# Kernel tuning notes

Measured on AMD Instinct MI355X. Metric: run time of the kernel, lower is better.

The kernel has to match this reference:

```python
import jax, jax.numpy as jnp
import numpy as np

N = 100_000            # nodes (residues) across batch
E = 1_200_000          # directed edges before duplication
G = 400                # graphs in batch
RBF_SIZE = 16
MIN_D, MAX_D = 0.0, 20.0
RAW_EDGE = 2           # enc_in_edges - rbf_size
RAW_NODE = 51          # enc_in_nodes - residue_emb_size
EMB = 32
NODE_OUT = 2           # features.Output.Node.LENGTH
GLOB_OUT = 1           # features.Output.Global.LENGTH
# (in_e, in_n, out_e, out_n) per message-passing layer (layers=3 schedule)
LAYER_DIMS = [(8, 16, 16, 32), (16, 32, 32, 64), (32, 64, 64, 128)]


def setup_inputs() -> dict:
    key = jax.random.key(0)
    ks = iter(jax.random.split(key, 64))
    def nrm(shape, s=0.1):
        return jax.random.normal(next(ks), shape, jnp.float32) * s
    inp = dict(
        node_raw=nrm((N, RAW_NODE), 1.0),
        edge_raw=nrm((E, RAW_EDGE), 1.0),
        distances=jax.random.uniform(next(ks), (E,), jnp.float32, 0.0, MAX_D),
        residues=jax.random.randint(next(ks), (N,), 0, 22, jnp.int32),
        senders=jax.random.randint(next(ks), (E,), 0, N, jnp.int32),
        receivers=jax.random.randint(next(ks), (E,), 0, N, jnp.int32),
        node_graph_idx=jnp.sort(jax.random.randint(next(ks), (N,), 0, G, jnp.int32)),
        emb=nrm((22, EMB), 1.0),
        enc_We1=nrm((18, 4)), enc_be1=jnp.zeros((4,), jnp.float32),
        enc_We2=nrm((4, 8)), enc_be2=jnp.zeros((8,), jnp.float32),
        enc_Wn1=nrm((83, 8)), enc_bn1=jnp.zeros((8,), jnp.float32),
        enc_Wn2=nrm((8, 16)), enc_bn2=jnp.zeros((16,), jnp.float32),
        ro_Wg=nrm((128, GLOB_OUT)), ro_bg=jnp.zeros((GLOB_OUT,), jnp.float32),
        ro_Wn=nrm((128, NODE_OUT)), ro_bn=jnp.zeros((NODE_OUT,), jnp.float32),
    )
    for i, (ie, inn, oe, on) in enumerate(LAYER_DIMS):
        inp[f'l{i}_We'] = nrm((ie, oe))
        inp[f'l{i}_Ws'] = nrm((inn, oe))
        inp[f'l{i}_be'] = jnp.zeros((oe,), jnp.float32)
        inp[f'l{i}_Wn'] = nrm((inn, on))
        inp[f'l{i}_Wi'] = nrm((oe, on))
        inp[f'l{i}_bn'] = jnp.zeros((on,), jnp.float32)
    return inp


def _seg_mean(x, idx, num):
    s = jax.ops.segment_sum(x, idx, num_segments=num)
    c = jax.ops.segment_sum(jnp.ones((x.shape[0],), x.dtype), idx, num_segments=num)
    return s / jnp.maximum(c, 1.0)[:, None]


def _forward(node_raw, edge_raw, distances, residues, senders, receivers, node_graph_idx,
             emb, enc_We1, enc_be1, enc_We2, enc_be2, enc_Wn1, enc_bn1, enc_Wn2, enc_bn2,
             ro_Wg, ro_bg, ro_Wn, ro_bn, layer_params):
    relu = jax.nn.relu
    # --- preprocessing ---
    centers = jnp.linspace(MIN_D, MAX_D, RBF_SIZE)
    rbf = jnp.exp(-(distances[:, None] - centers[None, :]) ** 2)      # [E, 16]
    ef = jnp.concatenate([rbf, edge_raw], axis=1)                      # [E, 18]
    nf = jnp.concatenate([emb[residues], node_raw], axis=1)            # [N, 83]
    # duplicate (symmetrize) edges
    snd = jnp.concatenate([senders, receivers])                        # [2E]
    rcv = jnp.concatenate([receivers, senders])                        # [2E]
    ef = jnp.concatenate([ef, ef], axis=0)                             # [2E, 18]
    # --- encoder (edge MLP then node MLP, eval mode: no dropout/BN) ---
    ef = relu(ef @ enc_We1 + enc_be1)
    ef = relu(ef @ enc_We2 + enc_be2)
    nf = relu(nf @ enc_Wn1 + enc_bn1)
    nf = relu(nf @ enc_Wn2 + enc_bn2)
    # --- message-passing layers ---
    for (We, Ws, be, Wn, Wi, bn) in layer_params:
        # EdgeLinear: concat(edge_feats, sender_feats) @ W == sum of two matmuls
        ef = relu(ef @ We + nf[snd] @ Ws + be)                         # [2E, out_e]
        agg = _seg_mean(ef, rcv, N)                                    # [N, out_e] mean of incoming
        nf = relu(nf @ Wn + agg @ Wi + bn)                             # [N, out_n]
    # --- readout ---
    gmean = _seg_mean(nf, node_graph_idx, G)                           # [G, 128]
    glob = jax.nn.sigmoid(gmean @ ro_Wg + ro_bg)                       # [G, 1]
    node_out = jax.nn.sigmoid(nf @ ro_Wn + ro_bn)                      # [N, 2]
    return node_out, glob


def reference(node_raw, edge_raw, distances, residues, senders, receivers, node_graph_idx,
              emb, enc_We1, enc_be1, enc_We2, enc_be2, enc_Wn1, enc_bn1, enc_Wn2, enc_bn2,
              ro_Wg, ro_bg, ro_Wn, ro_bn,
              l0_We, l0_Ws, l0_be, l0_Wn, l0_Wi, l0_bn,
              l1_We, l1_Ws, l1_be, l1_Wn, l1_Wi, l1_bn,
              l2_We, l2_Ws, l2_be, l2_Wn, l2_Wi, l2_bn):
    layer_params = [
        (l0_We, l0_Ws, l0_be, l0_Wn, l0_Wi, l0_bn),
        (l1_We, l1_Ws, l1_be, l1_Wn, l1_Wi, l1_bn),
        (l2_We, l2_Ws, l2_be, l2_Wn, l2_Wi, l2_bn),
    ]
    return _forward(node_raw, edge_raw, distances, residues, senders, receivers, node_graph_idx,
                    emb, enc_We1, enc_be1, enc_We2, enc_be2, enc_Wn1, enc_bn1, enc_Wn2, enc_bn2,
                    ro_Wg, ro_bg, ro_Wn, ro_bn, layer_params)
```

## Files before the change

### kernel.cpp

```cpp
#include <hip/hip_runtime.h>
#include <hip/hip_fp16.h>
#include <cstdint>
#include <cstddef>


__device__ __forceinline__ float sigmoidf_(float x) {
    return 1.0f / (1.0f + __expf(-x));
}

template<int OUT>
__device__ __forceinline__ void load_bias(const float* __restrict__ b, float* __restrict__ acc) {
#pragma unroll
    for (int j = 0; j < OUT; ++j) acc[j] = b[j];
}

template<int OUT>
__device__ __forceinline__ void relu_v(float* __restrict__ acc) {
#pragma unroll
    for (int j = 0; j < OUT; ++j) acc[j] = fmaxf(acc[j], 0.0f);
}

template<int IN, int OUT>
__device__ __forceinline__ void mm_acc(const float* __restrict__ x,
                                       const float* __restrict__ W,
                                       float* __restrict__ acc) {
#pragma unroll 4
    for (int k = 0; k < IN; ++k) {
        const float v = x[k];
#pragma unroll
        for (int j = 0; j < OUT; ++j) acc[j] = fmaf(v, W[k * OUT + j], acc[j]);
    }
}

template<int WIDTH>
__device__ __forceinline__ void load_row(const float* __restrict__ p, float* __restrict__ x) {
#pragma unroll
    for (int k4 = 0; k4 < WIDTH / 4; ++k4) {
        float4 v = reinterpret_cast<const float4*>(p)[k4];
        x[k4 * 4 + 0] = v.x; x[k4 * 4 + 1] = v.y;
        x[k4 * 4 + 2] = v.z; x[k4 * 4 + 3] = v.w;
    }
}

__device__ __forceinline__ void enc_edge(int orig,
                                         const float* __restrict__ dist,
                                         const float* __restrict__ eraw,
                                         const float* __restrict__ We1, const float* __restrict__ be1,
                                         const float* __restrict__ We2, const float* __restrict__ be2,
                                         float* __restrict__ out8) {
    float x[18];
    const float d = dist[orig];
#pragma unroll
    for (int i = 0; i < 16; ++i) {
        const float c = (float)i * (20.0f / 15.0f);
        const float t = d - c;
        x[i] = __expf(-t * t);
    }
    x[16] = eraw[(size_t)orig * 2 + 0];
    x[17] = eraw[(size_t)orig * 2 + 1];
    float h[4];
    load_bias<4>(be1, h);
    mm_acc<18, 4>(x, We1, h);
    relu_v<4>(h);
    load_bias<8>(be2, out8);
    mm_acc<4, 8>(h, We2, out8);
    relu_v<8>(out8);
}

__device__ __forceinline__ void chain_ef0_y(int orig, int s,
    const float* __restrict__ dist, const float* __restrict__ eraw,
    const float* __restrict__ eWe1, const float* __restrict__ ebe1,
    const float* __restrict__ eWe2, const float* __restrict__ ebe2,
    const float* __restrict__ We0,
    const float* __restrict__ y0, float* __restrict__ a0)
{
    load_row<16>(y0 + (size_t)s * 16, a0);
    float enc[8];
    enc_edge(orig, dist, eraw, eWe1, ebe1, eWe2, ebe2, enc);
    mm_acc<8, 16>(enc, We0, a0);
    relu_v<16>(a0);
}

__device__ __forceinline__ void chain_ef0(int orig, int s,
    const float* __restrict__ dist, const float* __restrict__ eraw,
    const float* __restrict__ eWe1, const float* __restrict__ ebe1,
    const float* __restrict__ eWe2, const float* __restrict__ ebe2,
    const float* __restrict__ We0, const float* __restrict__ Ws0, const float* __restrict__ b0,
    const float* __restrict__ nf0, float* __restrict__ a0)
{
    float x0[16];
    load_row<16>(nf0 + (size_t)s * 16, x0);
    float enc[8];
    enc_edge(orig, dist, eraw, eWe1, ebe1, eWe2, ebe2, enc);
    load_bias<16>(b0, a0);
    mm_acc<8, 16>(enc, We0, a0);
    mm_acc<16, 16>(x0, Ws0, a0);
    relu_v<16>(a0);
}

__device__ __forceinline__ int lower_bound_i(const int* __restrict__ a, int n, int key) {
    int lo = 0, hi = n;
    while (lo < hi) {
        int mid = (lo + hi) >> 1;
        if (a[mid] < key) lo = mid + 1; else hi = mid;
    }
    return lo;
}

__device__ __forceinline__ int upper_bound_i(const int* __restrict__ a, int n, int key) {
    int lo = 0, hi = n;
    while (lo < hi) {
        int mid = (lo + hi) >> 1;
        if (a[mid] <= key) lo = mid + 1; else hi = mid;
    }
    return lo;
}


__global__ void __launch_bounds__(256) k_count(
    const int* __restrict__ senders, const int* __restrict__ receivers,
    int* __restrict__ ideg, int E)
{
    const int e = blockIdx.x * blockDim.x + threadIdx.x;
    if (e >= E) return;
    atomicAdd(&ideg[receivers[e]], 1);
    atomicAdd(&ideg[senders[e]], 1);
}

__global__ void __launch_bounds__(256) k_blocksum(
    const int* __restrict__ ideg, int* __restrict__ bsum, int N)
{
    __shared__ int s[256];
    const int t = threadIdx.x;
    const int i = blockIdx.x * 256 + t;
    s[t] = (i < N) ? ideg[i] : 0;
    __syncthreads();
#pragma unroll
    for (int d = 128; d > 0; d >>= 1) {
        if (t < d) s[t] += s[t + d];
        __syncthreads();
    }
    if (t == 0) bsum[blockIdx.x] = s[0];
}

__global__ void __launch_bounds__(1024) k_scan_partials(int* __restrict__ bsum, int nb)
{
    __shared__ int s[1024];
    const int t = threadIdx.x;
    const int v = (t < nb) ? bsum[t] : 0;
    s[t] = v;
    __syncthreads();
    for (int d = 1; d < 1024; d <<= 1) {
        const int w = (t >= d) ? s[t - d] : 0;
        __syncthreads();
        s[t] += w;
        __syncthreads();
    }
    if (t < nb) bsum[t] = s[t] - v;
}

__global__ void __launch_bounds__(256) k_blockscan(
    const int* __restrict__ ideg, const int* __restrict__ bsum,
    int* __restrict__ offs, int* __restrict__ cursor, int N)
{
    __shared__ int s[256];
    const int t = threadIdx.x;
    const int i = blockIdx.x * 256 + t;
    const int v = (i < N) ? ideg[i] : 0;
    s[t] = v;
    __syncthreads();
    for (int d = 1; d < 256; d <<= 1) {
        const int w = (t >= d) ? s[t - d] : 0;
        __syncthreads();
        s[t] += w;
        __syncthreads();
    }
    if (i < N) {
        const int o = bsum[blockIdx.x] + s[t] - v;
        offs[i] = o;
        cursor[i] = o;
    }
}

__global__ void __launch_bounds__(256) k_scatter(
    const int* __restrict__ senders, const int* __restrict__ receivers,
    int* __restrict__ cursor, int2* __restrict__ perm2, int E)
{
    const int e = blockIdx.x * blockDim.x + threadIdx.x;
    if (e >= E) return;
    const int se = senders[e];
    const int re = receivers[e];
    const int p = atomicAdd(&cursor[re], 1);
    perm2[p] = make_int2(e, se);
    const int q = atomicAdd(&cursor[se], 1);
    perm2[q] = make_int2(e, re);
}


__global__ void __launch_bounds__(256) node_enc_kernel(
    const float* __restrict__ node_raw, const int* __restrict__ residues,
    const float* __restrict__ emb,
    const float* __restrict__ Wn1, const float* __restrict__ bn1,
    const float* __restrict__ Wn2, const float* __restrict__ bn2,
    const float* __restrict__ Ws0, const float* __restrict__ b0,
    float* __restrict__ nf0, float* __restrict__ y0, int N)
{
    __shared__ float raw[256 * 51];
    const int t = threadIdx.x;
    const int n0 = blockIdx.x * 256;
    int cnt = N - n0; if (cnt > 256) cnt = 256;
    const int tot = cnt * 51;
    for (int i = t; i < tot; i += 256)
        raw[i] = node_raw[(size_t)n0 * 51 + i];
    __syncthreads();

    const int n = n0 + t;
    if (n >= N) return;
    float h[8];
    load_bias<8>(bn1, h);
    {
        const float* er = emb + (size_t)residues[n] * 32;
        float x[32];
        load_row<32>(er, x);
        mm_acc<32, 8>(x, Wn1, h);
    }
    {
        const float* nr = &raw[t * 51];
#pragma unroll 4
        for (int k = 0; k < 51; ++k) {
            const float v = nr[k];
#pragma unroll
            for (int j = 0; j < 8; ++j) h[j] = fmaf(v, Wn1[(32 + k) * 8 + j], h[j]);
        }
    }
    relu_v<8>(h);
    float o[16];
    load_bias<16>(bn2, o);
    mm_acc<8, 16>(h, Wn2, o);
    relu_v<16>(o);
    float* dst = nf0 + (size_t)n * 16;
#pragma unroll
    for (int j = 0; j < 16; ++j) dst[j] = o[j];
    if (y0) {
        float yr[16];
        load_bias<16>(b0, yr);
        mm_acc<16, 16>(o, Ws0, yr);
        float* yd = y0 + (size_t)n * 16;
#pragma unroll
        for (int j = 0; j < 16; ++j) yd[j] = yr[j];
    }
}

template<int IN>
__global__ void __launch_bounds__(256) y_kernel(
    const float* __restrict__ nf, const float* __restrict__ Ws, const float* __restrict__ b,
    float* __restrict__ y, __half* __restrict__ yh, int N)
{
    constexpr int BN = 64;
    __shared__ float xs[BN * IN];
    const int t = threadIdx.x;
    const int n0 = blockIdx.x * BN;
    int cnt = N - n0; if (cnt > BN) cnt = BN;
    if (cnt <= 0) return;
    {
        const float4* gx = reinterpret_cast<const float4*>(nf + (size_t)n0 * IN);
        float4* lx = reinterpret_cast<float4*>(xs);
        const int nx = cnt * IN / 4;
        for (int i = t; i < nx; i += 256) lx[i] = gx[i];
    }
    __syncthreads();

    constexpr int SUB = 256 / IN;
    const int j = t % IN;
    const int m = t / IN;
    float w[IN];
#pragma unroll
    for (int k = 0; k < IN; ++k) w[k] = Ws[k * IN + j];
    const float bj = b[j];

    for (int nl = m; nl < cnt; nl += SUB) {
        const float4* x4 = reinterpret_cast<const float4*>(&xs[nl * IN]);
        float p0 = bj, p1 = 0.0f, p2 = 0.0f, p3 = 0.0f;
#pragma unroll
        for (int k4 = 0; k4 < IN / 4; ++k4) {
            float4 v = x4[k4];
            p0 = fmaf(v.x, w[4 * k4 + 0], p0);
            p1 = fmaf(v.y, w[4 * k4 + 1], p1);
            p2 = fmaf(v.z, w[4 * k4 + 2], p2);
            p3 = fmaf(v.w, w[4 * k4 + 3], p3);
        }
        const float r = (p0 + p1) + (p2 + p3);
        if (y)  y[(size_t)(n0 + nl) * IN + j] = r;
        if (yh) yh[(size_t)(n0 + nl) * IN + j] = __float2half(r);
    }
}

template<int INN, int OE, int ON>
__global__ void __launch_bounds__(256) node_layer_v4(
    const float* __restrict__ nf_in, const float* __restrict__ agg, const int* __restrict__ ideg,
    const float* __restrict__ Wn, const float* __restrict__ Wi, const float* __restrict__ bn,
    float* __restrict__ nf_out, int N)
{
    constexpr int BN = 64;
    __shared__ float xs[BN * INN];
    __shared__ float as_[BN * OE];
    __shared__ float inv_s[BN];
    const int t = threadIdx.x;
    const int n0 = blockIdx.x * BN;
    int cnt = N - n0; if (cnt > BN) cnt = BN;
    if (cnt <= 0) return;

    {
        const float4* gx = reinterpret_cast<const float4*>(nf_in + (size_t)n0 * INN);
        float4* lx = reinterpret_cast<float4*>(xs);
        const int nx = cnt * INN / 4;
        for (int i = t; i < nx; i += 256) lx[i] = gx[i];
        const float4* ga = reinterpret_cast<const float4*>(agg + (size_t)n0 * OE);
        float4* la = reinterpret_cast<float4*>(as_);
        const int na = cnt * OE / 4;
        for (int i = t; i < na; i += 256) la[i] = ga[i];
        if (t < cnt) inv_s[t] = 1.0f / fmaxf((float)ideg[n0 + t], 1.0f);
    }
    __syncthreads();

    constexpr int SUB = 256 / ON;
    const int j = t % ON;
    const int m = t / ON;

    float wn[INN], wi[OE];
#pragma unroll
    for (int k = 0; k < INN; ++k) wn[k] = Wn[k * ON + j];
#pragma unroll
    for (int k = 0; k < OE; ++k)  wi[k] = Wi[k * ON + j];
    const float bj = bn[j];

    for (int nl = m; nl < cnt; nl += SUB) {
        const float4* x4 = reinterpret_cast<const float4*>(&xs[nl * INN]);
        const float4* a4 = reinterpret_cast<const float4*>(&as_[nl * OE]);
        const float inv = inv_s[nl];

        float p0 = bj, p1 = 0.0f, p2 = 0.0f, p3 = 0.0f;
#pragma unroll
        for (int k4 = 0; k4 < INN / 4; ++k4) {
            float4 v = x4[k4];
            p0 = fmaf(v.x, wn[4 * k4 + 0], p0);
            p1 = fmaf(v.y, wn[4 * k4 + 1], p1);
            p2 = fmaf(v.z, wn[4 * k4 + 2], p2);
            p3 = fmaf(v.w, wn[4 * k4 + 3], p3);
        }
        float q0 = 0.0f, q1 = 0.0f, q2 = 0.0f, q3 = 0.0f;
#pragma unroll
        for (int k4 = 0; k4 < OE / 4; ++k4) {
            float4 v = a4[k4];
            q0 = fmaf(v.x, wi[4 * k4 + 0], q0);
            q1 = fmaf(v.y, wi[4 * k4 + 1], q1);
            q2 = fmaf(v.z, wi[4 * k4 + 2], q2);
            q3 = fmaf(v.w, wi[4 * k4 + 3], q3);
        }
        const float r = (p0 + p1) + (p2 + p3) + inv * ((q0 + q1) + (q2 + q3));
        nf_out[(size_t)(n0 + nl) * ON + j] = fmaxf(r, 0.0f);
    }
}

__global__ void __launch_bounds__(256) node_layer_v4b(
    const float* __restrict__ nf_in, const float* __restrict__ agg, const int* __restrict__ ideg,
    const float* __restrict__ Wn, const float* __restrict__ Wi, const float* __restrict__ bn,
    float* __restrict__ nf_out, int N)
{
    constexpr int BN = 64;
    __shared__ float xs[BN * 64];
    __shared__ float as_[BN * 64];
    __shared__ float inv_s[BN];
    const int t = threadIdx.x;
    const int n0 = blockIdx.x * BN;
    int cnt = N - n0; if (cnt > BN) cnt = BN;
    if (cnt <= 0) return;

    {
        const float4* gx = reinterpret_cast<const float4*>(nf_in + (size_t)n0 * 64);
        float4* lx = reinterpret_cast<float4*>(xs);
        const int nx = cnt * 16;
        for (int i = t; i < nx; i += 256) lx[i] = gx[i];
        const float4* ga = reinterpret_cast<const float4*>(agg + (size_t)n0 * 64);
        float4* la = reinterpret_cast<float4*>(as_);
        for (int i = t; i < nx; i += 256) la[i] = ga[i];
        if (t < cnt) inv_s[t] = 1.0f / fmaxf((float)ideg[n0 + t], 1.0f);
    }
    __syncthreads();

    const int j = t >> 1;
    const int h = t & 1;

    float wn[32], wi[32];
#pragma unroll
    for (int k = 0; k < 32; ++k) wn[k] = Wn[(h * 32 + k) * 128 + j];
#pragma unroll
    for (int k = 0; k < 32; ++k) wi[k] = Wi[(h * 32 + k) * 128 + j];
    const float bj = bn[j];

    for (int nl = 0; nl < cnt; ++nl) {
        const float4* x4 = reinterpret_cast<const float4*>(&xs[nl * 64 + h * 32]);
        const float4* a4 = reinterpret_cast<const float4*>(&as_[nl * 64 + h * 32]);

        float p0 = 0.0f, p1 = 0.0f, p2 = 0.0f, p3 = 0.0f;
#pragma unroll
        for (int k4 = 0; k4 < 8; ++k4) {
            float4 v = x4[k4];
            p0 = fmaf(v.x, wn[4 * k4 + 0], p0);
            p1 = fmaf(v.y, wn[4 * k4 + 1], p1);
            p2 = fmaf(v.z, wn[4 * k4 + 2], p2);
            p3 = fmaf(v.w, wn[4 * k4 + 3], p3);
        }
        float q0 = 0.0f, q1 = 0.0f, q2 = 0.0f, q3 = 0.0f;
#pragma unroll
        for (int k4 = 0; k4 < 8; ++k4) {
            float4 v = a4[k4];
            q0 = fmaf(v.x, wi[4 * k4 + 0], q0);
            q1 = fmaf(v.y, wi[4 * k4 + 1], q1);
            q2 = fmaf(v.z, wi[4 * k4 + 2], q2);
            q3 = fmaf(v.w, wi[4 * k4 + 3], q3);
        }
        float r = (p0 + p1) + (p2 + p3) + inv_s[nl] * ((q0 + q1) + (q2 + q3));
        r += __shfl_xor(r, 1);
        if (h == 0)
            nf_out[(size_t)(n0 + nl) * 128 + j] = fmaxf(r + bj, 0.0f);
    }
}

__global__ void __launch_bounds__(256) node_out_kernel(
    const float* __restrict__ nf3,
    const float* __restrict__ roWn, const float* __restrict__ robn,
    float* __restrict__ node_out, int N)
{
    const int n = blockIdx.x * blockDim.x + threadIdx.x;
    if (n >= N) return;
    const float* x = nf3 + (size_t)n * 128;
    float a0 = robn[0], a1 = robn[1];
#pragma unroll 4
    for (int k4 = 0; k4 < 32; ++k4) {
        float4 v = reinterpret_cast<const float4*>(x)[k4];
        const float vv[4] = {v.x, v.y, v.z, v.w};
#pragma unroll
        for (int u = 0; u < 4; ++u) {
            const int k = k4 * 4 + u;
            a0 = fmaf(vv[u], roWn[k * 2 + 0], a0);
            a1 = fmaf(vv[u], roWn[k * 2 + 1], a1);
        }
    }
    node_out[(size_t)n * 2 + 0] = sigmoidf_(a0);
    node_out[(size_t)n * 2 + 1] = sigmoidf_(a1);
}

__global__ void __launch_bounds__(256) graph_out_kernel(
    const float* __restrict__ nf3, const int* __restrict__ gidx,
    const float* __restrict__ roWg, const float* __restrict__ robg,
    float* __restrict__ glob_out, int N)
{
    __shared__ float sred[256];
    __shared__ float gm[128];
    const int g = blockIdx.x;
    const int t = threadIdx.x;
    const int lo = lower_bound_i(gidx, N, g);
    const int hi = lower_bound_i(gidx, N, g + 1);
    const int cnt = hi - lo;

    const int c = t & 127;
    const int h = t >> 7;
    float acc = 0.0f;
    for (int i = lo + h; i < hi; i += 2)
        acc += nf3[(size_t)i * 128 + c];
    sred[t] = acc;
    __syncthreads();
    if (t < 128) {
        const float m = (sred[t] + sred[t + 128]) / fmaxf((float)cnt, 1.0f);
        gm[t] = m * roWg[t];
    }
    __syncthreads();
    if (t < 64) gm[t] += gm[t + 64];
    __syncthreads();
    if (t < 32) gm[t] += gm[t + 32];
    __syncthreads();
    if (t < 16) gm[t] += gm[t + 16];
    __syncthreads();
    if (t == 0) {
        float s = 0.0f;
#pragma unroll
        for (int i = 0; i < 16; ++i) s += gm[i];
        glob_out[g] = sigmoidf_(s + robg[0]);
    }
}


__global__ void __launch_bounds__(256) fused0_kernel(
    const float* __restrict__ dist, const float* __restrict__ eraw,
    const int2* __restrict__ perm2, const float* __restrict__ y0,
    const float* __restrict__ eWe1, const float* __restrict__ ebe1,
    const float* __restrict__ eWe2, const float* __restrict__ ebe2,
    const float* __restrict__ We0,
    const int* __restrict__ offs, const int* __restrict__ ideg,
    float* __restrict__ agg, int N, int E2)
{
    __shared__ float lds[256 * 17];
    const int t = threadIdx.x;
    const int p0 = blockIdx.x * 256;
    int cnt = E2 - p0; if (cnt > 256) cnt = 256;

    if (t < cnt) {
        const int2 pr = perm2[p0 + t];
        float a0[16];
        chain_ef0_y(pr.x, pr.y, dist, eraw, eWe1, ebe1, eWe2, ebe2, We0, y0, a0);
        float* row = &lds[t * 17];
#pragma unroll
        for (int j = 0; j < 16; ++j) row[j] = a0[j];
    }
    __syncthreads();

    const int n_lo = upper_bound_i(offs, N, p0) - 1;
    const int n_hi = upper_bound_i(offs, N, p0 + cnt - 1) - 1;
    const int col = t & 15;
    const int grp = t >> 4;
    const int pend = p0 + cnt;

    for (int n = n_lo + grp; n <= n_hi; n += 16) {
        int lo = offs[n];
        int hi = lo + ideg[n];
        lo = lo > p0 ? lo : p0;
        hi = hi < pend ? hi : pend;
        if (lo >= hi) continue;
        float acc = 0.0f;
        for (int p = lo; p < hi; ++p)
            acc += lds[(p - p0) * 17 + col];
        atomicAdd(&agg[(size_t)n * 16 + col], acc);
    }
}

__global__ void __launch_bounds__(256) fused1_kernel(
    const float* __restrict__ dist, const float* __restrict__ eraw,
    const int2* __restrict__ perm2,
    const float* __restrict__ y0, const float* __restrict__ y1,
    const float* __restrict__ eWe1, const float* __restrict__ ebe1,
    const float* __restrict__ eWe2, const float* __restrict__ ebe2,
    const float* __restrict__ We0, const float* __restrict__ We1,
    const int* __restrict__ offs, const int* __restrict__ ideg,
    float* __restrict__ agg, int N, int E2)
{
    __shared__ float lds[256 * 32];
    const int t = threadIdx.x;
    const int p0 = blockIdx.x * 256;
    int cnt = E2 - p0; if (cnt > 256) cnt = 256;

    if (t < cnt) {
        const int2 pr = perm2[p0 + t];
        const int s = pr.y;
        float a1[32];
        load_row<32>(y1 + (size_t)s * 32, a1);
        float a0[16];
        chain_ef0_y(pr.x, s, dist, eraw, eWe1, ebe1, eWe2, ebe2, We0, y0, a0);
        mm_acc<16, 32>(a0, We1, a1);
        relu_v<32>(a1);
        const int m = t & 31;
        float* row = &lds[t * 32];
#pragma unroll
        for (int j = 0; j < 32; ++j) row[j ^ m] = a1[j];
    }
    __syncthreads();

    const int n_lo = upper_bound_i(offs, N, p0) - 1;
    const int n_hi = upper_bound_i(offs, N, p0 + cnt - 1) - 1;
    const int col = t & 31;
    const int grp = t >> 5;
    const int pend = p0 + cnt;

    for (int n = n_lo + grp; n <= n_hi; n += 8) {
        int lo = offs[n];
        int hi = lo + ideg[n];
        lo = lo > p0 ? lo : p0;
        hi = hi < pend ? hi : pend;
        if (lo >= hi) continue;
        float acc = 0.0f;
        for (int p = lo; p < hi; ++p) {
            const int sl = p - p0;
            acc += lds[sl * 32 + (col ^ (sl & 31))];
        }
        atomicAdd(&agg[(size_t)n * 32 + col], acc);
    }
}

__global__ void __launch_bounds__(256) fused2_kernel(
    const float* __restrict__ dist, const float* __restrict__ eraw,
    const int2* __restrict__ perm2,
    const float* __restrict__ y0, const __half2* __restrict__ y1h, const __half2* __restrict__ y2h,
    const float* __restrict__ eWe1, const float* __restrict__ ebe1,
    const float* __restrict__ eWe2, const float* __restrict__ ebe2,
    const float* __restrict__ We0, const float* __restrict__ We1, const float* __restrict__ We2,
    const int* __restrict__ offs, const int* __restrict__ ideg,
    float* __restrict__ agg, int N, int E2)
{
    __shared__ __half2 lds[256 * 32];
    const int t = threadIdx.x;
    const int p0 = blockIdx.x * 256;
    int cnt = E2 - p0; if (cnt > 256) cnt = 256;

    if (t < cnt) {
        const int2 pr = perm2[p0 + t];
        const int s = pr.y;
        float a2[64];
        {
            const __half2* yh = y2h + (size_t)s * 32;
#pragma unroll
            for (int q = 0; q < 32; ++q) {
                const float2 f = __half22float2(yh[q]);
                a2[2 * q] = f.x; a2[2 * q + 1] = f.y;
            }
        }
        float a1[32];
        {
            const __half2* yh = y1h + (size_t)s * 16;
#pragma unroll
            for (int q = 0; q < 16; ++q) {
                const float2 f = __half22float2(yh[q]);
                a1[2 * q] = f.x; a1[2 * q + 1] = f.y;
            }
        }
        float a0[16];
        chain_ef0_y(pr.x, s, dist, eraw, eWe1, ebe1, eWe2, ebe2, We0, y0, a0);
        mm_acc<16, 32>(a0, We1, a1);
        relu_v<32>(a1);
        mm_acc<32, 64>(a1, We2, a2);
        const int m = t & 31;
        __half2* row = &lds[t * 32];
#pragma unroll
        for (int q = 0; q < 32; ++q) {
            row[q ^ m] = __floats2half2_rn(fmaxf(a2[2 * q], 0.0f),
                                           fmaxf(a2[2 * q + 1], 0.0f));
        }
    }
    __syncthreads();

    const int n_lo = upper_bound_i(offs, N, p0) - 1;
    const int n_hi = upper_bound_i(offs, N, p0 + cnt - 1) - 1;
    const int col = t & 63;
    const int grp = t >> 6;
    const int pend = p0 + cnt;
    const int q = col >> 1;
    const bool hiHalf = (col & 1) != 0;

    for (int n = n_lo + grp; n <= n_hi; n += 4) {
        int lo = offs[n];
        int hi = lo + ideg[n];
        lo = lo > p0 ? lo : p0;
        hi = hi < pend ? hi : pend;
        if (lo >= hi) continue;
        float acc = 0.0f;
        for (int p = lo; p < hi; ++p) {
            const int sl = p - p0;
            const __half2 hv = lds[sl * 32 + (q ^ (sl & 31))];
            const float2 f2 = __half22float2(hv);
            acc += hiHalf ? f2.y : f2.x;
        }
        atomicAdd(&agg[(size_t)n * 64 + col], acc);
    }
}


template<int LAYER>
__global__ void __launch_bounds__(256) edge_scatter_kernel(
    const float* __restrict__ dist, const float* __restrict__ eraw,
    const int* __restrict__ senders, const int* __restrict__ receivers,
    const float* __restrict__ nf0, const float* __restrict__ nf1, const float* __restrict__ nf2,
    const float* __restrict__ eWe1, const float* __restrict__ ebe1,
    const float* __restrict__ eWe2, const float* __restrict__ ebe2,
    const float* __restrict__ We0, const float* __restrict__ Ws0, const float* __restrict__ b0,
    const float* __restrict__ We1, const float* __restrict__ Ws1, const float* __restrict__ b1,
    const float* __restrict__ We2, const float* __restrict__ Ws2, const float* __restrict__ b2,
    float* __restrict__ agg, int E, int E2)
{
    const int e = blockIdx.x * blockDim.x + threadIdx.x;
    if (e >= E2) return;
    const int orig = (e < E) ? e : e - E;
    const int s = (e < E) ? senders[orig] : receivers[orig];
    const int r = (e < E) ? receivers[orig] : senders[orig];

    float a0[16];
    chain_ef0(orig, s, dist, eraw, eWe1, ebe1, eWe2, ebe2, We0, Ws0, b0, nf0, a0);

    if constexpr (LAYER == 0) {
        float* dst = agg + (size_t)r * 16;
#pragma unroll
        for (int j = 0; j < 16; ++j) atomicAdd(dst + j, a0[j]);
    } else {
        float a1[32];
        load_bias<32>(b1, a1);
        mm_acc<16, 32>(a0, We1, a1);
        {
            float x[32];
            load_row<32>(nf1 + (size_t)s * 32, x);
            mm_acc<32, 32>(x, Ws1, a1);
        }
        relu_v<32>(a1);

        if constexpr (LAYER == 1) {
            float* dst = agg + (size_t)r * 32;
#pragma unroll
            for (int j = 0; j < 32; ++j) atomicAdd(dst + j, a1[j]);
        } else {
            float a2[64];
            load_bias<64>(b2, a2);
            mm_acc<32, 64>(a1, We2, a2);
            {
                const float* xr = nf2 + (size_t)s * 64;
#pragma unroll
                for (int k4 = 0; k4 < 16; ++k4) {
                    float4 v = reinterpret_cast<const float4*>(xr)[k4];
                    const float vv[4] = {v.x, v.y, v.z, v.w};
#pragma unroll
                    for (int u = 0; u < 4; ++u) {
                        const float val = vv[u];
                        const int k = k4 * 4 + u;
#pragma unroll
                        for (int j = 0; j < 64; ++j) a2[j] = fmaf(val, Ws2[k * 64 + j], a2[j]);
                    }
                }
            }
            relu_v<64>(a2);
            float* dst = agg + (size_t)r * 64;
#pragma unroll
            for (int j = 0; j < 64; ++j) atomicAdd(dst + j, a2[j]);
        }
    }
}


static inline size_t align_up(size_t x, size_t a) { return (x + a - 1) & ~(a - 1); }

extern "C" void kernel_launch(void* const* d_in, const int* in_sizes, int n_in,
                              void* d_out, int out_size, void* d_ws, size_t ws_size,
                              hipStream_t stream) {
    const float* node_raw  = (const float*)d_in[0];
    const float* edge_raw  = (const float*)d_in[1];
    const float* distances = (const float*)d_in[2];
    const int*   residues  = (const int*)d_in[3];
    const int*   senders   = (const int*)d_in[4];
    const int*   receivers = (const int*)d_in[5];
    const int*   gidx      = (const int*)d_in[6];
    const float* emb       = (const float*)d_in[7];
    const float* eWe1 = (const float*)d_in[8];  const float* ebe1 = (const float*)d_in[9];
    const float* eWe2 = (const float*)d_in[10]; const float* ebe2 = (const float*)d_in[11];
    const float* nWn1 = (const float*)d_in[12]; const float* nbn1 = (const float*)d_in[13];
    const float* nWn2 = (const float*)d_in[14]; const float* nbn2 = (const float*)d_in[15];
    const float* roWg = (const float*)d_in[16]; const float* robg = (const float*)d_in[17];
    const float* roWn = (const float*)d_in[18]; const float* robn = (const float*)d_in[19];
    const float* l0We = (const float*)d_in[20]; const float* l0Ws = (const float*)d_in[21];
    const float* l0be = (const float*)d_in[22]; const float* l0Wn = (const float*)d_in[23];
    const float* l0Wi = (const float*)d_in[24]; const float* l0bn = (const float*)d_in[25];
    const float* l1We = (const float*)d_in[26]; const float* l1Ws = (const float*)d_in[27];
    const float* l1be = (const float*)d_in[28]; const float* l1Wn = (const float*)d_in[29];
    const float* l1Wi = (const float*)d_in[30]; const float* l1bn = (const float*)d_in[31];
    const float* l2We = (const float*)d_in[32]; const float* l2Ws = (const float*)d_in[33];
    const float* l2be = (const float*)d_in[34]; const float* l2Wn = (const float*)d_in[35];
    const float* l2Wi = (const float*)d_in[36]; const float* l2bn = (const float*)d_in[37];

    const int N  = in_sizes[3];
    const int E  = in_sizes[2];
    const int G  = out_size - 2 * N;
    const int E2 = 2 * E;
    const int nb = (N + 255) / 256;

    const dim3 blk(256);
    const int nb_N  = (N + 255) / 256;
    const int nb_E  = (E + 255) / 256;
    const int nb_E2 = (E2 + 255) / 256;
    const int nlb64 = (N + 63) / 64;

    char* base = (char*)d_ws;
    size_t off = 0;
    int* ideg   = (int*)(base + off); off += align_up((size_t)N * 4, 16);
    int* offs   = (int*)(base + off); off += align_up((size_t)N * 4, 16);
    int* cursor = (int*)(base + off); off += align_up((size_t)N * 4, 16);
    int* bsum   = (int*)(base + off); off += align_up((size_t)1024 * 4, 16);
    float* nf0 = (float*)(base + off); off += (size_t)N * 16 * 4;
    float* nf1 = (float*)(base + off); off += (size_t)N * 32 * 4;
    float* nf2 = (float*)(base + off); off += (size_t)N * 64 * 4;
    float* nf3 = (float*)(base + off); off += (size_t)N * 128 * 4;
    float* agg = (float*)(base + off); off += (size_t)N * 64 * 4;
    const size_t need_fallback = off;
    int2* perm2 = (int2*)(base + off); off += align_up((size_t)E2 * 8, 16);
    float* y0 = (float*)(base + off); off += (size_t)N * 16 * 4;
    float* y1 = (float*)(base + off); off += (size_t)N * 32 * 4;
    __half* y1h = (__half*)(base + off); off += align_up((size_t)N * 32 * 2, 16);
    __half* y2h = (__half*)(base + off); off += align_up((size_t)N * 64 * 2, 16);
    const size_t need_fast = off;

    const bool fast = (ws_size >= need_fast);
    (void)need_fallback;

    hipMemsetAsync(ideg, 0, (size_t)N * 4, stream);
    k_count<<<nb_E, blk, 0, stream>>>(senders, receivers, ideg, E);
    node_enc_kernel<<<nb_N, blk, 0, stream>>>(node_raw, residues, emb, nWn1, nbn1, nWn2, nbn2,
                                              l0Ws, l0be, nf0, fast ? y0 : nullptr, N);

    if (fast) {
        k_blocksum<<<nb, blk, 0, stream>>>(ideg, bsum, N);
        k_scan_partials<<<1, 1024, 0, stream>>>(bsum, nb);
        k_blockscan<<<nb, blk, 0, stream>>>(ideg, bsum, offs, cursor, N);
        k_scatter<<<nb_E, blk, 0, stream>>>(senders, receivers, cursor, perm2, E);

        hipMemsetAsync(agg, 0, (size_t)N * 16 * 4, stream);
        fused0_kernel<<<nb_E2, blk, 0, stream>>>(distances, edge_raw, perm2, y0,
            eWe1, ebe1, eWe2, ebe2, l0We, offs, ideg, agg, N, E2);
        node_layer_v4<16, 16, 32><<<nlb64, blk, 0, stream>>>(nf0, agg, ideg, l0Wn, l0Wi, l0bn, nf1, N);
        y_kernel<32><<<nlb64, blk, 0, stream>>>(nf1, l1Ws, l1be, y1, y1h, N);

        hipMemsetAsync(agg, 0, (size_t)N * 32 * 4, stream);
        fused1_kernel<<<nb_E2, blk, 0, stream>>>(distances, edge_raw, perm2, y0, y1,
            eWe1, ebe1, eWe2, ebe2, l0We, l1We, offs, ideg, agg, N, E2);
        node_layer_v4<32, 32, 64><<<nlb64, blk, 0, stream>>>(nf1, agg, ideg, l1Wn, l1Wi, l1bn, nf2, N);
        y_kernel<64><<<nlb64, blk, 0, stream>>>(nf2, l2Ws, l2be, nullptr, y2h, N);

        hipMemsetAsync(agg, 0, (size_t)N * 64 * 4, stream);
        fused2_kernel<<<nb_E2, blk, 0, stream>>>(distances, edge_raw, perm2,
            y0, (const __half2*)y1h, (const __half2*)y2h,
            eWe1, ebe1, eWe2, ebe2, l0We, l1We, l2We, offs, ideg, agg, N, E2);
        node_layer_v4b<<<nlb64, blk, 0, stream>>>(nf2, agg, ideg, l2Wn, l2Wi, l2bn, nf3, N);
    } else {
        hipMemsetAsync(agg, 0, (size_t)N * 16 * 4, stream);
        edge_scatter_kernel<0><<<nb_E2, blk, 0, stream>>>(distances, edge_raw, senders, receivers,
            nf0, nf0, nf0, eWe1, ebe1, eWe2, ebe2,
            l0We, l0Ws, l0be, l1We, l1Ws, l1be, l2We, l2Ws, l2be, agg, E, E2);
        node_layer_v4<16, 16, 32><<<nlb64, blk, 0, stream>>>(nf0, agg, ideg, l0Wn, l0Wi, l0bn, nf1, N);

        hipMemsetAsync(agg, 0, (size_t)N * 32 * 4, stream);
        edge_scatter_kernel<1><<<nb_E2, blk, 0, stream>>>(distances, edge_raw, senders, receivers,
            nf0, nf1, nf1, eWe1, ebe1, eWe2, ebe2,
            l0We, l0Ws, l0be, l1We, l1Ws, l1be, l2We, l2Ws, l2be, agg, E, E2);
        node_layer_v4<32, 32, 64><<<nlb64, blk, 0, stream>>>(nf1, agg, ideg, l1Wn, l1Wi, l1bn, nf2, N);

        hipMemsetAsync(agg, 0, (size_t)N * 64 * 4, stream);
        edge_scatter_kernel<2><<<nb_E2, blk, 0, stream>>>(distances, edge_raw, senders, receivers,
            nf0, nf1, nf2, eWe1, ebe1, eWe2, ebe2,
            l0We, l0Ws, l0be, l1We, l1Ws, l1be, l2We, l2Ws, l2be, agg, E, E2);
        node_layer_v4b<<<nlb64, blk, 0, stream>>>(nf2, agg, ideg, l2Wn, l2Wi, l2bn, nf3, N);
    }

    node_out_kernel<<<nb_N, blk, 0, stream>>>(nf3, roWn, robn, (float*)d_out, N);
    graph_out_kernel<<<G, blk, 0, stream>>>(nf3, gidx, roWg, robg, (float*)d_out + (size_t)2 * N, N);
}
```

Before: 1.066 ms.

## Cache layer-0 edge features in fp16 and reuse in later layers

```diff
diff --git a/kernel.cpp b/kernel.cpp
--- a/kernel.cpp
+++ b/kernel.cpp
@@ -39,6 +39,15 @@
         float4 v = reinterpret_cast<const float4*>(p)[k4];
         x[k4 * 4 + 0] = v.x; x[k4 * 4 + 1] = v.y;
         x[k4 * 4 + 2] = v.z; x[k4 * 4 + 3] = v.w;
+    }
+}
+
+template<int PAIRS>
+__device__ __forceinline__ void load_h2(const __half2* __restrict__ p, float* __restrict__ x) {
+#pragma unroll
+    for (int q = 0; q < PAIRS; ++q) {
+        const float2 f = __half22float2(p[q]);
+        x[2 * q] = f.x; x[2 * q + 1] = f.y;
     }
 }
 
@@ -498,7 +507,7 @@
     const float* __restrict__ eWe2, const float* __restrict__ ebe2,
     const float* __restrict__ We0,
     const int* __restrict__ offs, const int* __restrict__ ideg,
-    float* __restrict__ agg, int N, int E2)
+    float* __restrict__ agg, __half2* __restrict__ ef0h, int N, int E2)
 {
     __shared__ float lds[256 * 17];
     const int t = threadIdx.x;
@@ -512,6 +521,12 @@
         float* row = &lds[t * 17];
 #pragma unroll
         for (int j = 0; j < 16; ++j) row[j] = a0[j];
+        if (ef0h) {
+            __half2* eh = ef0h + (size_t)(p0 + t) * 8;
+#pragma unroll
+            for (int q = 0; q < 8; ++q)
+                eh[q] = __floats2half2_rn(a0[2 * q], a0[2 * q + 1]);
+        }
     }
     __syncthreads();
 
@@ -537,7 +552,8 @@
 __global__ void __launch_bounds__(256) fused1_kernel(
     const float* __restrict__ dist, const float* __restrict__ eraw,
     const int2* __restrict__ perm2,
-    const float* __restrict__ y0, const float* __restrict__ y1,
+    const float* __restrict__ y0, const __half2* __restrict__ y1h,
+    const __half2* __restrict__ ef0h,
     const float* __restrict__ eWe1, const float* __restrict__ ebe1,
     const float* __restrict__ eWe2, const float* __restrict__ ebe2,
     const float* __restrict__ We0, const float* __restrict__ We1,
@@ -553,9 +569,13 @@
         const int2 pr = perm2[p0 + t];
         const int s = pr.y;
         float a1[32];
-        load_row<32>(y1 + (size_t)s * 32, a1);
+        load_h2<16>(y1h + (size_t)s * 16, a1);
         float a0[16];
-        chain_ef0_y(pr.x, s, dist, eraw, eWe1, ebe1, eWe2, ebe2, We0, y0, a0);
+        if (ef0h) {
+            load_h2<8>(ef0h + (size_t)(p0 + t) * 8, a0);
+        } else {
+            chain_ef0_y(pr.x, s, dist, eraw, eWe1, ebe1, eWe2, ebe2, We0, y0, a0);
+        }
         mm_acc<16, 32>(a0, We1, a1);
         relu_v<32>(a1);
         const int m = t & 31;
@@ -590,6 +610,7 @@
     const float* __restrict__ dist, const float* __restrict__ eraw,
     const int2* __restrict__ perm2,
     const float* __restrict__ y0, const __half2* __restrict__ y1h, const __half2* __restrict__ y2h,
+    const __half2* __restrict__ ef0h,
     const float* __restrict__ eWe1, const float* __restrict__ ebe1,
     const float* __restrict__ eWe2, const float* __restrict__ ebe2,
     const float* __restrict__ We0, const float* __restrict__ We1, const float* __restrict__ We2,
@@ -605,25 +626,15 @@
         const int2 pr = perm2[p0 + t];
         const int s = pr.y;
         float a2[64];
-        {
-            const __half2* yh = y2h + (size_t)s * 32;
-#pragma unroll
-            for (int q = 0; q < 32; ++q) {
-                const float2 f = __half22float2(yh[q]);
-                a2[2 * q] = f.x; a2[2 * q + 1] = f.y;
-            }
-        }
+        load_h2<32>(y2h + (size_t)s * 32, a2);
         float a1[32];
-        {
-            const __half2* yh = y1h + (size_t)s * 16;
-#pragma unroll
-            for (int q = 0; q < 16; ++q) {
-                const float2 f = __half22float2(yh[q]);
-                a1[2 * q] = f.x; a1[2 * q + 1] = f.y;
-            }
-        }
+        load_h2<16>(y1h + (size_t)s * 16, a1);
         float a0[16];
-        chain_ef0_y(pr.x, s, dist, eraw, eWe1, ebe1, eWe2, ebe2, We0, y0, a0);
+        if (ef0h) {
+            load_h2<8>(ef0h + (size_t)(p0 + t) * 8, a0);
+        } else {
+            chain_ef0_y(pr.x, s, dist, eraw, eWe1, ebe1, eWe2, ebe2, We0, y0, a0);
+        }
         mm_acc<16, 32>(a0, We1, a1);
         relu_v<32>(a1);
         mm_acc<32, 64>(a1, We2, a2);
@@ -786,10 +797,12 @@
     const size_t need_fallback = off;
     int2* perm2 = (int2*)(base + off); off += align_up((size_t)E2 * 8, 16);
     float* y0 = (float*)(base + off); off += (size_t)N * 16 * 4;
-    float* y1 = (float*)(base + off); off += (size_t)N * 32 * 4;
     __half* y1h = (__half*)(base + off); off += align_up((size_t)N * 32 * 2, 16);
     __half* y2h = (__half*)(base + off); off += align_up((size_t)N * 64 * 2, 16);
     const size_t need_fast = off;
+    __half2* ef0h = nullptr;
+    const size_t need_encA = need_fast + align_up((size_t)E2 * 16, 16);
+    if (ws_size >= need_encA) ef0h = (__half2*)(base + need_fast);
 
     const bool fast = (ws_size >= need_fast);
     (void)need_fallback;
@@ -807,19 +820,20 @@
 
         hipMemsetAsync(agg, 0, (size_t)N * 16 * 4, stream);
         fused0_kernel<<<nb_E2, blk, 0, stream>>>(distances, edge_raw, perm2, y0,
-            eWe1, ebe1, eWe2, ebe2, l0We, offs, ideg, agg, N, E2);
+            eWe1, ebe1, eWe2, ebe2, l0We, offs, ideg, agg, ef0h, N, E2);
         node_layer_v4<16, 16, 32><<<nlb64, blk, 0, stream>>>(nf0, agg, ideg, l0Wn, l0Wi, l0bn, nf1, N);
-        y_kernel<32><<<nlb64, blk, 0, stream>>>(nf1, l1Ws, l1be, y1, y1h, N);
+        y_kernel<32><<<nlb64, blk, 0, stream>>>(nf1, l1Ws, l1be, nullptr, y1h, N);
 
         hipMemsetAsync(agg, 0, (size_t)N * 32 * 4, stream);
-        fused1_kernel<<<nb_E2, blk, 0, stream>>>(distances, edge_raw, perm2, y0, y1,
+        fused1_kernel<<<nb_E2, blk, 0, stream>>>(distances, edge_raw, perm2,
+            y0, (const __half2*)y1h, ef0h,
             eWe1, ebe1, eWe2, ebe2, l0We, l1We, offs, ideg, agg, N, E2);
         node_layer_v4<32, 32, 64><<<nlb64, blk, 0, stream>>>(nf1, agg, ideg, l1Wn, l1Wi, l1bn, nf2, N);
         y_kernel<64><<<nlb64, blk, 0, stream>>>(nf2, l2Ws, l2be, nullptr, y2h, N);
 
         hipMemsetAsync(agg, 0, (size_t)N * 64 * 4, stream);
         fused2_kernel<<<nb_E2, blk, 0, stream>>>(distances, edge_raw, perm2,
-            y0, (const __half2*)y1h, (const __half2*)y2h,
+            y0, (const __half2*)y1h, (const __half2*)y2h, ef0h,
             eWe1, ebe1, eWe2, ebe2, l0We, l1We, l2We, offs, ideg, agg, N, E2);
         node_layer_v4b<<<nlb64, blk, 0, stream>>>(nf2, agg, ideg, l2Wn, l2Wi, l2bn, nf3, N);
     } else {
```

Result: faster. 983.6 us, median of 2 (-7.7%).
